# Optimization experiments

Measured on AMD Instinct MI355X. Metric: run time of the kernel, lower is better.

Reference implementation:

```python
import jax, jax.numpy as jnp
import numpy as np


def _to_complex(x):
    return x[..., 0] + 1j * x[..., 1]


def setup_inputs() -> dict:
    key = jax.random.key(0)
    ks = jax.random.split(key, 4)
    Bsz, L, D, N = 4, 16384, 512, 64
    u = jax.random.normal(ks[0], (Bsz, L, D), dtype=jnp.float32)
    # DPLR HiPPO-like init: real part -0.5, spread imaginary parts
    lam_re = -0.5 * jnp.ones((N,), jnp.float32)
    lam_im = jnp.pi * jnp.arange(N, dtype=jnp.float32)
    Lambda_ri = jnp.stack([lam_re, lam_im], axis=-1)              # (N, 2)
    P_ri = 0.5 * jax.random.normal(ks[1], (N, 2), jnp.float32)    # (N, 2)
    B_ri = 0.5 * jax.random.normal(ks[2], (N, D, 2), jnp.float32) # (N, D, 2)
    C_ri = (1.0 / np.float32(np.sqrt(N))) * jax.random.normal(ks[3], (1, N, 2), jnp.float32)
    D_param = jnp.ones((1,), jnp.float32)
    log_step = jnp.log(jnp.full((1,), 0.01, dtype=jnp.float32))
    return {"u": u, "Lambda_ri": Lambda_ri, "P_ri": P_ri, "B_ri": B_ri,
            "C_ri": C_ri, "D_param": D_param, "log_step": log_step}


def reference(u, Lambda_ri, P_ri, B_ri, C_ri, D_param, log_step):
    # Reassemble complex parameters (torch stores them via view_as_real)
    Lambda = _to_complex(Lambda_ri)   # (N,)
    P = _to_complex(P_ri)             # (N,)  (Q = P in S4Base)
    Bm = _to_complex(B_ri)            # (N, D)
    C = _to_complex(C_ri)             # (1, N)
    L = u.shape[-2]
    step = jnp.exp(log_step)[0]

    # --- conv_kernel_DPLR: Cauchy-kernel generating function at roots of unity ---
    Omega = jnp.exp((-2j * jnp.pi / L) * jnp.arange(L))          # (L,)
    g = (2.0 / step) * ((1.0 - Omega) / (1.0 + Omega))           # (L,)
    cauchy = 1.0 / (g[:, None] - Lambda[None, :])                # (L, N)
    aC = jnp.conj(C)[0]                                          # (N,)
    qc = jnp.conj(P)                                             # (N,)
    # k00[l,d] = sum_n C*[n] B[n,d] / (g[l]-Lambda[n]), etc.
    k00 = jnp.einsum('n,nd,ln->ld', aC, Bm, cauchy)              # (L, D)
    k01 = cauchy @ (aC * P)                                      # (L,)
    k10 = jnp.einsum('n,nd,ln->ld', qc, Bm, cauchy)              # (L, D)
    k11 = cauchy @ (qc * P)                                      # (L,)
    evaluated = (2.0 / (1.0 + Omega))[:, None] * (
        k00 - k01[:, None] * (1.0 / (1.0 + k11))[:, None] * k10)  # (L, D)
    K = jnp.fft.ifft(evaluated, n=L, axis=0).real                # (L, D) real kernel

    # --- convolve: FFT convolution over the sequence axis (zero-padded to 2L) ---
    n_fft = 2 * L
    ud = jnp.fft.rfft(u, n=n_fft, axis=-2)                       # (B, L+1..., D) complex
    Kd = jnp.fft.rfft(K, n=n_fft, axis=0)                        # (L+1..., D)
    y = jnp.fft.irfft(ud * Kd, n=n_fft, axis=-2)[..., :L, :]     # (B, L, D)
    return y + D_param * u
```

## Files before the change

kernel.cpp:

```cpp
#include <hip/hip_runtime.h>
#include <math.h>


#define D_DIM 512
#define NFFT 16384
#define TWO_PI_F 6.283185307179586f
#define PI_F 3.14159265358979323846f

struct C2 { float x, y; };

__device__ __forceinline__ C2 cmul(C2 a, C2 b){ return C2{a.x*b.x - a.y*b.y, a.x*b.y + a.y*b.x}; }
__device__ __forceinline__ C2 cadd(C2 a, C2 b){ return C2{a.x+b.x, a.y+b.y}; }
__device__ __forceinline__ C2 csub(C2 a, C2 b){ return C2{a.x-b.x, a.y-b.y}; }
__device__ __forceinline__ C2 cdiv(C2 a, C2 b){
  float inv = 1.f/(b.x*b.x + b.y*b.y);
  return C2{(a.x*b.x + a.y*b.y)*inv, (a.y*b.x - a.x*b.y)*inv};
}
__device__ __forceinline__ void cfma_(C2& acc, C2 a, C2 b){
  acc.x = fmaf(a.x, b.x, fmaf(-a.y, b.y, acc.x));
  acc.y = fmaf(a.x, b.y, fmaf( a.y, b.x, acc.y));
}

template<bool INV>
__device__ __forceinline__ void dft4(C2& a, C2& b, C2& c, C2& d){
  C2 t0 = cadd(a,c), t1 = csub(a,c), t2 = cadd(b,d), t3 = csub(b,d);
  C2 it3 = INV ? C2{-t3.y, t3.x} : C2{t3.y, -t3.x};
  a = cadd(t0,t2); c = csub(t0,t2); b = cadd(t1,it3); d = csub(t1,it3);
}

template<bool INV>
__device__ __forceinline__ void twd(C2& v, float c, float s){
  C2 w{c, INV ? s : -s};
  v = cmul(v, w);
}

template<bool INV>
__device__ __forceinline__ void dft16(C2 v[16]){
  dft4<INV>(v[0], v[4], v[8],  v[12]);
  dft4<INV>(v[1], v[5], v[9],  v[13]);
  dft4<INV>(v[2], v[6], v[10], v[14]);
  dft4<INV>(v[3], v[7], v[11], v[15]);
  const float C1 = 0.9238795325112867f, S1 = 0.3826834323650898f;
  const float CQ = 0.7071067811865476f;
  const float C3 = 0.3826834323650898f, S3 = 0.9238795325112867f;
  twd<INV>(v[5],  C1,  S1);
  twd<INV>(v[9],  CQ,  CQ);
  twd<INV>(v[13], C3,  S3);
  twd<INV>(v[6],  CQ,  CQ);
  twd<INV>(v[10], 0.f, 1.f);
  twd<INV>(v[14], -CQ, CQ);
  twd<INV>(v[7],  C3,  S3);
  twd<INV>(v[11], -CQ, CQ);
  twd<INV>(v[15], -C1, -S1);
  dft4<INV>(v[0],  v[1],  v[2],  v[3]);
  dft4<INV>(v[4],  v[5],  v[6],  v[7]);
  dft4<INV>(v[8],  v[9],  v[10], v[11]);
  dft4<INV>(v[12], v[13], v[14], v[15]);
}

template<bool INV>
__device__ __forceinline__ void dft8(C2 v[8]){
  C2 e0=v[0], e1=v[2], e2=v[4], e3=v[6];
  C2 o0=v[1], o1=v[3], o2=v[5], o3=v[7];
  dft4<INV>(e0,e1,e2,e3);
  dft4<INV>(o0,o1,o2,o3);
  const float r = 0.7071067811865476f;
  C2 w1 = INV ? C2{r, r}    : C2{r, -r};
  C2 w2 = INV ? C2{0.f,1.f} : C2{0.f,-1.f};
  C2 w3 = INV ? C2{-r, r}   : C2{-r, -r};
  C2 t0=o0, t1=cmul(o1,w1), t2=cmul(o2,w2), t3=cmul(o3,w3);
  v[0]=cadd(e0,t0); v[4]=csub(e0,t0);
  v[1]=cadd(e1,t1); v[5]=csub(e1,t1);
  v[2]=cadd(e2,t2); v[6]=csub(e2,t2);
  v[3]=cadd(e3,t3); v[7]=csub(e3,t3);
}

template<bool INV, bool PACK>
__global__ __launch_bounds__(256) void k_sweep1(const void* __restrict__ srcv, C2* __restrict__ out,
                                                long long src_bstride, long long out_bstride){
  __shared__ C2 V[128*32];
  int bx = blockIdx.x;
  int a  = bx & 127;
  int dt = bx >> 7;
  int tid = threadIdx.x;
  int dl = tid & 31;
  int g  = tid >> 5;
  int d0 = dt*32 + dl;
  const float sgn = INV ? 1.f : -1.f;
  C2* ob = out + (long long)blockIdx.y * out_bstride;

  #pragma unroll
  for (int h=0; h<2; ++h){
    int j1 = 2*g + h;
    C2 v[8];
    if constexpr (PACK){
      const float* sb = (const float*)srcv + (long long)blockIdx.y * src_bstride;
      #pragma unroll
      for (int j2=0;j2<4;j2++){
        int rr = a + 128*(j1 + 16*j2);
        v[j2].x = sb[(long long)(2*rr)  *D_DIM + d0];
        v[j2].y = sb[(long long)(2*rr+1)*D_DIM + d0];
      }
      #pragma unroll
      for (int j2=4;j2<8;j2++) v[j2] = C2{0.f,0.f};
    } else {
      const C2* sb = (const C2*)srcv + (long long)blockIdx.y * src_bstride;
      #pragma unroll
      for (int j2=0;j2<8;j2++){
        int rr = a + 128*(j1 + 16*j2);
        v[j2] = sb[(long long)rr*D_DIM + d0];
      }
    }
    dft8<INV>(v);
    float sn, cs; __sincosf(sgn * TWO_PI_F * (float)j1 * (1.f/128.f), &sn, &cs);
    C2 w1{cs, sn}; C2 w = w1;
    #pragma unroll
    for (int k2=1;k2<8;k2++){ v[k2] = cmul(v[k2], w); w = cmul(w, w1); }
    #pragma unroll
    for (int k2=0;k2<8;k2++) V[(k2*16 + j1)*32 + dl] = v[k2];
  }
  __syncthreads();
  C2 y[16];
  #pragma unroll
  for (int j1=0;j1<16;j1++) y[j1] = V[(g*16 + j1)*32 + dl];
  dft16<INV>(y);
  float sb_, cb_; __sincosf(sgn * TWO_PI_F * (float)(a*g) * (1.f/16384.f), &sb_, &cb_);
  float ss_, cs2; __sincosf(sgn * TWO_PI_F * (float)(8*a)  * (1.f/16384.f), &ss_, &cs2);
  C2 tw{cb_, sb_}; C2 stp{cs2, ss_};
  #pragma unroll
  for (int k1=0;k1<16;k1++){
    int pidx = ((k1&3)<<2) | (k1>>2);
    C2 val = cmul(y[pidx], tw);
    int k2p = g + 8*k1;
    ob[(long long)(k2p*128 + a)*D_DIM + d0] = val;
    tw = cmul(tw, stp);
  }
}

template<bool INV, int OMODE>
__global__ __launch_bounds__(256) void k_sweep2(const C2* __restrict__ in, void* __restrict__ outv,
                                                const float* __restrict__ u, const float* __restrict__ Dp,
                                                long long in_bstride, long long out_bstride){
  __shared__ C2 V[128*32];
  int bx = blockIdx.x;
  int a  = bx & 127;
  int dt = bx >> 7;
  int tid = threadIdx.x;
  int dl = tid & 31;
  int g  = tid >> 5;
  int d0 = dt*32 + dl;
  const float sgn = INV ? 1.f : -1.f;
  const C2* ib = in + (long long)blockIdx.y * in_bstride;

  #pragma unroll
  for (int h=0; h<2; ++h){
    int j1 = 2*g + h;
    C2 v[8];
    #pragma unroll
    for (int j2=0;j2<8;j2++){
      int rr = a*128 + (j1 + 16*j2);
      v[j2] = ib[(long long)rr*D_DIM + d0];
    }
    dft8<INV>(v);
    float sn, cs; __sincosf(sgn * TWO_PI_F * (float)j1 * (1.f/128.f), &sn, &cs);
    C2 w1{cs, sn}; C2 w = w1;
    #pragma unroll
    for (int k2=1;k2<8;k2++){ v[k2] = cmul(v[k2], w); w = cmul(w, w1); }
    #pragma unroll
    for (int k2=0;k2<8;k2++) V[(k2*16 + j1)*32 + dl] = v[k2];
  }
  __syncthreads();
  C2 y[16];
  #pragma unroll
  for (int j1=0;j1<16;j1++) y[j1] = V[(g*16 + j1)*32 + dl];
  dft16<INV>(y);
  #pragma unroll
  for (int k1=0;k1<16;k1++){
    int pidx = ((k1&3)<<2) | (k1>>2);
    C2 val = y[pidx];
    int row = a + 128*(g + 8*k1);
    if constexpr (OMODE == 0){
      C2* ob = (C2*)outv + (long long)blockIdx.y * out_bstride;
      ob[(long long)row*D_DIM + d0] = val;
    } else if constexpr (OMODE == 1){
      float* ob = (float*)outv;
      ob[(long long)row*D_DIM + d0] = val.x;
    } else {
      if (row < 8192){
        float* yb = (float*)outv + (long long)blockIdx.y * out_bstride;
        const float* ub = u + (long long)blockIdx.y * out_bstride;
        float dp = Dp[0];
        const float invN = 1.f/16384.f;
        yb[(long long)(2*row)  *D_DIM + d0] = fmaf(dp, ub[(long long)(2*row)  *D_DIM + d0], val.x*invN);
        yb[(long long)(2*row+1)*D_DIM + d0] = fmaf(dp, ub[(long long)(2*row+1)*D_DIM + d0], val.y*invN);
      }
    }
  }
}

__global__ __launch_bounds__(256) void k_mul(const C2* __restrict__ Zu, const C2* __restrict__ ZK,
                                             C2* __restrict__ Zp, long long bstride){
  int idx = blockIdx.x*256 + threadIdx.x;
  int d = idx & (D_DIM-1);
  int k = idx >> 9;
  int m = (NFFT - k) & (NFFT - 1);
  const C2* zub = Zu + (long long)blockIdx.y * bstride;
  C2*       zpb = Zp + (long long)blockIdx.y * bstride;
  C2 a  = zub[(long long)k*D_DIM + d];
  C2 bm = zub[(long long)m*D_DIM + d];
  C2 hk = ZK [(long long)k*D_DIM + d];
  C2 hm = ZK [(long long)m*D_DIM + d];
  float sw, cw; __sincosf(PI_F * (float)k / 16384.f, &sw, &cw);
  C2 w  { cw, -sw};
  C2 wm {-cw, -sw};
  C2 Ze  {0.5f*(a.x + bm.x), 0.5f*(a.y - bm.y)};
  C2 Zo  {0.5f*(a.y + bm.y), -0.5f*(a.x - bm.x)};
  C2 Xk = cadd(Ze, cmul(w, Zo));
  C2 Zem {0.5f*(bm.x + a.x), 0.5f*(bm.y - a.y)};
  C2 Zom {0.5f*(bm.y + a.y), -0.5f*(bm.x - a.x)};
  C2 Xm = cadd(Zem, cmul(wm, Zom));
  C2 KZe  {0.5f*(hk.x + hm.x), 0.5f*(hk.y - hm.y)};
  C2 KZo  {0.5f*(hk.y + hm.y), -0.5f*(hk.x - hm.x)};
  C2 Hk = cadd(KZe, cmul(w, KZo));
  C2 KZem {0.5f*(hm.x + hk.x), 0.5f*(hm.y - hk.y)};
  C2 KZom {0.5f*(hm.y + hk.y), -0.5f*(hm.x - hk.x)};
  C2 Hm = cadd(KZem, cmul(wm, KZom));
  C2 Yk = cmul(Xk, Hk);
  C2 Ym = cmul(Xm, Hm);
  C2 E  {0.5f*(Yk.x + Ym.x), 0.5f*(Yk.y - Ym.y)};
  C2 T  {0.5f*(Yk.x - Ym.x), 0.5f*(Yk.y + Ym.y)};
  C2 wp { cw, sw};
  C2 O = cmul(wp, T);
  zpb[(long long)k*D_DIM + d] = C2{E.x - O.y, E.y + O.x};
  if (k > 0 && k < 8192){
    C2 Em {0.5f*(Ym.x + Yk.x), 0.5f*(Ym.y - Yk.y)};
    C2 T2 {0.5f*(Ym.x - Yk.x), 0.5f*(Ym.y + Yk.y)};
    C2 wq {-cw, sw};
    C2 Om = cmul(wq, T2);
    zpb[(long long)m*D_DIM + d] = C2{Em.x - Om.y, Em.y + Om.x};
  }
}

__global__ __launch_bounds__(256) void k_prep(const float* __restrict__ B_ri, const float* __restrict__ C_ri,
                                              const float* __restrict__ P_ri,
                                              C2* __restrict__ U0, C2* __restrict__ U1, C2* __restrict__ vecs){
  int idx = blockIdx.x*256 + threadIdx.x;
  int n = idx >> 9;
  C2 Bnd { B_ri[2*idx], B_ri[2*idx+1] };
  C2 Cc  { C_ri[2*n], -C_ri[2*n+1] };
  C2 Pc  { P_ri[2*n], -P_ri[2*n+1] };
  U0[idx] = cmul(Cc, Bnd);
  U1[idx] = cmul(Pc, Bnd);
  if ((idx & (D_DIM-1)) == 0){
    C2 Pn { P_ri[2*n], P_ri[2*n+1] };
    vecs[n]       = cmul(Cc, Pn);
    vecs[64 + n]  = cmul(Pc, Pn);
  }
}

__global__ __launch_bounds__(256) void k_wprep(const float* __restrict__ Lambda_ri,
                                               const float* __restrict__ log_step,
                                               const C2* __restrict__ vecs,
                                               C2* __restrict__ Wbuf){
  __shared__ C2 p01[4][64];
  __shared__ C2 p11[4][64];
  __shared__ C2 sA1[64];
  int tid = threadIdx.x;
  int li = tid & 63, q = tid >> 6;
  int l = blockIdx.x*64 + li;
  float step = expf(log_step[0]);
  float ang = -TWO_PI_F * (float)l / 16384.f;
  float sn, cs; sincosf(ang, &sn, &cs);
  C2 den{1.f+cs, sn};
  C2 num{1.f-cs, -sn};
  C2 r = cdiv(num, den);
  float s2 = 2.f/step;
  C2 gl{r.x*s2, r.y*s2};
  C2 alpha = cdiv(C2{2.f/16384.f, 0.f}, den);
  C2 c[16]; C2 k01{0,0}, k11{0,0};
  #pragma unroll
  for (int i=0;i<16;i++){
    int n = q*16+i;
    C2 lam{Lambda_ri[2*n], Lambda_ri[2*n+1]};
    c[i] = cdiv(C2{1.f,0.f}, C2{gl.x-lam.x, gl.y-lam.y});
    cfma_(k01, c[i], vecs[n]);
    cfma_(k11, c[i], vecs[64+n]);
  }
  p01[q][li] = k01; p11[q][li] = k11;
  __syncthreads();
  if (q==0){
    C2 s01 = cadd(cadd(p01[0][li],p01[1][li]),cadd(p01[2][li],p01[3][li]));
    C2 s11 = cadd(cadd(p11[0][li],p11[1][li]),cadd(p11[2][li],p11[3][li]));
    C2 beta = cdiv(s01, C2{1.f+s11.x, s11.y});
    C2 ab = cmul(alpha, beta);
    sA1[li] = C2{-ab.x, -ab.y};
  }
  __syncthreads();
  C2 A1 = sA1[li];
  size_t base = (size_t)(l>>4)*(128*16) + (size_t)(l&15);
  #pragma unroll
  for (int i=0;i<16;i++){
    int n = q*16+i;
    Wbuf[base + (size_t)n*16]      = cmul(alpha, c[i]);
    Wbuf[base + (size_t)(64+n)*16] = cmul(A1, c[i]);
  }
}

__global__ __launch_bounds__(256) void k_ev2(const C2* __restrict__ U, const C2* __restrict__ Wbuf,
                                             C2* __restrict__ ev){
  int tid = threadIdx.x;
  int tile = blockIdx.x;
  int d0 = tid, d1 = tid + 256;
  const C2* __restrict__ Wt = Wbuf + (size_t)tile*(128*16);
  C2 acc0[16], acc1[16];
  #pragma unroll
  for (int li=0;li<16;li++){ acc0[li]=C2{0.f,0.f}; acc1[li]=C2{0.f,0.f}; }
  C2 u0 = U[d0], u1 = U[d1];
  for (int np=0; np<128; ++np){
    C2 nu0 = U[(size_t)(np+1)*D_DIM + d0];
    C2 nu1 = U[(size_t)(np+1)*D_DIM + d1];
    const C2* wr = Wt + (size_t)np*16;
    #pragma unroll
    for (int li=0;li<16;li++){
      C2 w = wr[li];
      cfma_(acc0[li], w, u0);
      cfma_(acc1[li], w, u1);
    }
    u0 = nu0; u1 = nu1;
  }
  long long l0 = (long long)tile*16;
  #pragma unroll
  for (int li=0;li<16;li++){
    ev[(l0+li)*D_DIM + d0] = acc0[li];
    ev[(l0+li)*D_DIM + d1] = acc1[li];
  }
}

extern "C" void kernel_launch(void* const* d_in, const int* in_sizes, int n_in,
                              void* d_out, int out_size, void* d_ws, size_t ws_size,
                              hipStream_t stream){
  const float* u         = (const float*)d_in[0];
  const float* Lambda_ri = (const float*)d_in[1];
  const float* P_ri      = (const float*)d_in[2];
  const float* B_ri      = (const float*)d_in[3];
  const float* C_ri      = (const float*)d_in[4];
  const float* Dp        = (const float*)d_in[5];
  const float* log_step  = (const float*)d_in[6];
  float* y = (float*)d_out;

  const long long ND = (long long)NFFT * D_DIM;
  const size_t SZ = (size_t)ND * sizeof(C2);

  int bc = 4;
  if (ws_size < (size_t)(2*4+1)*SZ) bc = 2;
  if (ws_size < (size_t)(2*2+1)*SZ) bc = 1;
  if (ws_size < (size_t)3*SZ) return;

  char* base = (char*)d_ws;
  C2* RA = (C2*)base;
  C2* RB = (C2*)(base + (size_t)bc*SZ);
  C2* RC = (C2*)(base + (size_t)2*bc*SZ);
  C2* Wbuf  = RC;
  float* Kreal = (float*)RC;
  C2* U0   = RB;
  C2* U1   = RB + 64*D_DIM;
  C2* vecs = RB + 2*64*D_DIM;
  C2* U    = RB;

  dim3 blk(256);

  k_prep <<<dim3(128),  blk, 0, stream>>>(B_ri, C_ri, P_ri, U0, U1, vecs);
  k_wprep<<<dim3(256),  blk, 0, stream>>>(Lambda_ri, log_step, vecs, Wbuf);
  k_ev2  <<<dim3(1024), blk, 0, stream>>>(U, Wbuf, RA);

  k_sweep1<true,false><<<dim3(2048,1), blk, 0, stream>>>(RA, RB, 0LL, 0LL);
  k_sweep2<true,1>    <<<dim3(2048,1), blk, 0, stream>>>(RB, Kreal, nullptr, nullptr, 0LL, 0LL);
  k_sweep1<false,true><<<dim3(2048,1), blk, 0, stream>>>(Kreal, RA, 0LL, 0LL);
  k_sweep2<false,0>   <<<dim3(2048,1), blk, 0, stream>>>(RA, RC, nullptr, nullptr, 0LL, 0LL);

  for (int b0 = 0; b0 < 4; b0 += bc){
    const float* ub = u + (long long)b0 * ND;
    float*       yb = y + (long long)b0 * ND;
    k_sweep1<false,true><<<dim3(2048,bc), blk, 0, stream>>>(ub, RA, ND, ND);
    k_sweep2<false,0>   <<<dim3(2048,bc), blk, 0, stream>>>(RA, RB, nullptr, nullptr, ND, ND);
    k_mul               <<<dim3(16386,bc), blk, 0, stream>>>(RB, RC, RA, ND);
    k_sweep1<true,false><<<dim3(2048,bc), blk, 0, stream>>>(RA, RB, ND, ND);
    k_sweep2<true,2>    <<<dim3(2048,bc), blk, 0, stream>>>(RB, yb, ub, Dp, ND, ND);
  }
}
```

Measured before the change: 845.8 us.

## Fuse spectral multiply into inverse FFT first pass; shrink ev2 L-tile

Removes the standalone k_mul kernel. Its real-FFT untangle and kernel multiply are now computed inside a new k_sweep1m kernel as it loads data for the inverse FFT's first pass, which saves a full round trip of the complex spectrum through global memory per batch. The cost is that each spectrum element's neighbour pair is read twice and the untangle arithmetic is done twice. Separately, the k_ev2 Cauchy evaluation tile shrinks from 16 to 8 sequence positions per block, with the grid doubled and the Wbuf layout in k_wprep changed to match, which halves accumulator registers for more occupancy at the cost of reading U twice as often.

```diff
diff --git a/kernel.cpp b/kernel.cpp
--- a/kernel.cpp
+++ b/kernel.cpp
@@ -137,6 +137,80 @@
   }
 }
 
+__global__ __launch_bounds__(256) void k_sweep1m(const C2* __restrict__ Zu, const C2* __restrict__ ZK,
+                                                 C2* __restrict__ out, long long bstride){
+  __shared__ C2 V[128*32];
+  int bx = blockIdx.x;
+  int a  = bx & 127;
+  int dt = bx >> 7;
+  int tid = threadIdx.x;
+  int dl = tid & 31;
+  int g  = tid >> 5;
+  int d0 = dt*32 + dl;
+  const C2* zub = Zu + (long long)blockIdx.y * bstride;
+  C2* ob = out + (long long)blockIdx.y * bstride;
+
+  #pragma unroll
+  for (int h=0; h<2; ++h){
+    int j1 = 2*g + h;
+    C2 v[8];
+    #pragma unroll
+    for (int j2=0;j2<8;j2++){
+      int rr = a + 128*(j1 + 16*j2);
+      int mr = (NFFT - rr) & (NFFT - 1);
+      C2 zk_ = zub[(long long)rr*D_DIM + d0];
+      C2 zm_ = zub[(long long)mr*D_DIM + d0];
+      C2 hk_ = ZK [(long long)rr*D_DIM + d0];
+      C2 hm_ = ZK [(long long)mr*D_DIM + d0];
+      float sw, cw; __sincosf(PI_F * (float)rr / 16384.f, &sw, &cw);
+      C2 w  { cw, -sw};
+      C2 wm {-cw, -sw};
+      C2 Ze  {0.5f*(zk_.x + zm_.x), 0.5f*(zk_.y - zm_.y)};
+      C2 Zo  {0.5f*(zk_.y + zm_.y), -0.5f*(zk_.x - zm_.x)};
+      C2 Xk = cadd(Ze, cmul(w, Zo));
+      C2 Zem {0.5f*(zm_.x + zk_.x), 0.5f*(zm_.y - zk_.y)};
+      C2 Zom {0.5f*(zm_.y + zk_.y), -0.5f*(zm_.x - zk_.x)};
+      C2 Xm = cadd(Zem, cmul(wm, Zom));
+      C2 KZe  {0.5f*(hk_.x + hm_.x), 0.5f*(hk_.y - hm_.y)};
+      C2 KZo  {0.5f*(hk_.y + hm_.y), -0.5f*(hk_.x - hm_.x)};
+      C2 Hk = cadd(KZe, cmul(w, KZo));
+      C2 KZem {0.5f*(hm_.x + hk_.x), 0.5f*(hm_.y - hk_.y)};
+      C2 KZom {0.5f*(hm_.y + hk_.y), -0.5f*(hm_.x - hk_.x)};
+      C2 Hm = cadd(KZem, cmul(wm, KZom));
+      C2 Yk = cmul(Xk, Hk);
+      C2 Ym = cmul(Xm, Hm);
+      C2 E  {0.5f*(Yk.x + Ym.x), 0.5f*(Yk.y - Ym.y)};
+      C2 T  {0.5f*(Yk.x - Ym.x), 0.5f*(Yk.y + Ym.y)};
+      C2 wp { cw, sw};
+      C2 O = cmul(wp, T);
+      v[j2] = C2{E.x - O.y, E.y + O.x};
+    }
+    dft8<true>(v);
+    float sn, cs; __sincosf(TWO_PI_F * (float)j1 * (1.f/128.f), &sn, &cs);
+    C2 w1{cs, sn}; C2 w = w1;
+    #pragma unroll
+    for (int k2=1;k2<8;k2++){ v[k2] = cmul(v[k2], w); w = cmul(w, w1); }
+    #pragma unroll
+    for (int k2=0;k2<8;k2++) V[(k2*16 + j1)*32 + dl] = v[k2];
+  }
+  __syncthreads();
+  C2 y[16];
+  #pragma unroll
+  for (int j1=0;j1<16;j1++) y[j1] = V[(g*16 + j1)*32 + dl];
+  dft16<true>(y);
+  float sb_, cb_; __sincosf(TWO_PI_F * (float)(a*g) * (1.f/16384.f), &sb_, &cb_);
+  float ss_, cs2; __sincosf(TWO_PI_F * (float)(8*a)  * (1.f/16384.f), &ss_, &cs2);
+  C2 tw{cb_, sb_}; C2 stp{cs2, ss_};
+  #pragma unroll
+  for (int k1=0;k1<16;k1++){
+    int pidx = ((k1&3)<<2) | (k1>>2);
+    C2 val = cmul(y[pidx], tw);
+    int k2p = g + 8*k1;
+    ob[(long long)(k2p*128 + a)*D_DIM + d0] = val;
+    tw = cmul(tw, stp);
+  }
+}
+
 template<bool INV, int OMODE>
 __global__ __launch_bounds__(256) void k_sweep2(const C2* __restrict__ in, void* __restrict__ outv,
                                                 const float* __restrict__ u, const float* __restrict__ Dp,
@@ -198,49 +272,6 @@
   }
 }
 
-__global__ __launch_bounds__(256) void k_mul(const C2* __restrict__ Zu, const C2* __restrict__ ZK,
-                                             C2* __restrict__ Zp, long long bstride){
-  int idx = blockIdx.x*256 + threadIdx.x;
-  int d = idx & (D_DIM-1);
-  int k = idx >> 9;
-  int m = (NFFT - k) & (NFFT - 1);
-  const C2* zub = Zu + (long long)blockIdx.y * bstride;
-  C2*       zpb = Zp + (long long)blockIdx.y * bstride;
-  C2 a  = zub[(long long)k*D_DIM + d];
-  C2 bm = zub[(long long)m*D_DIM + d];
-  C2 hk = ZK [(long long)k*D_DIM + d];
-  C2 hm = ZK [(long long)m*D_DIM + d];
-  float sw, cw; __sincosf(PI_F * (float)k / 16384.f, &sw, &cw);
-  C2 w  { cw, -sw};
-  C2 wm {-cw, -sw};
-  C2 Ze  {0.5f*(a.x + bm.x), 0.5f*(a.y - bm.y)};
-  C2 Zo  {0.5f*(a.y + bm.y), -0.5f*(a.x - bm.x)};
-  C2 Xk = cadd(Ze, cmul(w, Zo));
-  C2 Zem {0.5f*(bm.x + a.x), 0.5f*(bm.y - a.y)};
-  C2 Zom {0.5f*(bm.y + a.y), -0.5f*(bm.x - a.x)};
-  C2 Xm = cadd(Zem, cmul(wm, Zom));
-  C2 KZe  {0.5f*(hk.x + hm.x), 0.5f*(hk.y - hm.y)};
-  C2 KZo  {0.5f*(hk.y + hm.y), -0.5f*(hk.x - hm.x)};
-  C2 Hk = cadd(KZe, cmul(w, KZo));
-  C2 KZem {0.5f*(hm.x + hk.x), 0.5f*(hm.y - hk.y)};
-  C2 KZom {0.5f*(hm.y + hk.y), -0.5f*(hm.x - hk.x)};
-  C2 Hm = cadd(KZem, cmul(wm, KZom));
-  C2 Yk = cmul(Xk, Hk);
-  C2 Ym = cmul(Xm, Hm);
-  C2 E  {0.5f*(Yk.x + Ym.x), 0.5f*(Yk.y - Ym.y)};
-  C2 T  {0.5f*(Yk.x - Ym.x), 0.5f*(Yk.y + Ym.y)};
-  C2 wp { cw, sw};
-  C2 O = cmul(wp, T);
-  zpb[(long long)k*D_DIM + d] = C2{E.x - O.y, E.y + O.x};
-  if (k > 0 && k < 8192){
-    C2 Em {0.5f*(Ym.x + Yk.x), 0.5f*(Ym.y - Yk.y)};
-    C2 T2 {0.5f*(Ym.x - Yk.x), 0.5f*(Ym.y + Yk.y)};
-    C2 wq {-cw, sw};
-    C2 Om = cmul(wq, T2);
-    zpb[(long long)m*D_DIM + d] = C2{Em.x - Om.y, Em.y + Om.x};
-  }
-}
-
 __global__ __launch_bounds__(256) void k_prep(const float* __restrict__ B_ri, const float* __restrict__ C_ri,
                                               const float* __restrict__ P_ri,
                                               C2* __restrict__ U0, C2* __restrict__ U1, C2* __restrict__ vecs){
@@ -297,12 +328,12 @@
   }
   __syncthreads();
   C2 A1 = sA1[li];
-  size_t base = (size_t)(l>>4)*(128*16) + (size_t)(l&15);
+  size_t base = (size_t)(l>>3)*(128*8) + (size_t)(l&7);
   #pragma unroll
   for (int i=0;i<16;i++){
     int n = q*16+i;
-    Wbuf[base + (size_t)n*16]      = cmul(alpha, c[i]);
-    Wbuf[base + (size_t)(64+n)*16] = cmul(A1, c[i]);
+    Wbuf[base + (size_t)n*8]      = cmul(alpha, c[i]);
+    Wbuf[base + (size_t)(64+n)*8] = cmul(A1, c[i]);
   }
 }
 
@@ -311,26 +342,26 @@
   int tid = threadIdx.x;
   int tile = blockIdx.x;
   int d0 = tid, d1 = tid + 256;
-  const C2* __restrict__ Wt = Wbuf + (size_t)tile*(128*16);
-  C2 acc0[16], acc1[16];
-  #pragma unroll
-  for (int li=0;li<16;li++){ acc0[li]=C2{0.f,0.f}; acc1[li]=C2{0.f,0.f}; }
+  const C2* __restrict__ Wt = Wbuf + (size_t)tile*(128*8);
+  C2 acc0[8], acc1[8];
+  #pragma unroll
+  for (int li=0;li<8;li++){ acc0[li]=C2{0.f,0.f}; acc1[li]=C2{0.f,0.f}; }
   C2 u0 = U[d0], u1 = U[d1];
   for (int np=0; np<128; ++np){
     C2 nu0 = U[(size_t)(np+1)*D_DIM + d0];
     C2 nu1 = U[(size_t)(np+1)*D_DIM + d1];
-    const C2* wr = Wt + (size_t)np*16;
-    #pragma unroll
-    for (int li=0;li<16;li++){
+    const C2* wr = Wt + (size_t)np*8;
+    #pragma unroll
+    for (int li=0;li<8;li++){
       C2 w = wr[li];
       cfma_(acc0[li], w, u0);
       cfma_(acc1[li], w, u1);
     }
     u0 = nu0; u1 = nu1;
   }
-  long long l0 = (long long)tile*16;
-  #pragma unroll
-  for (int li=0;li<16;li++){
+  long long l0 = (long long)tile*8;
+  #pragma unroll
+  for (int li=0;li<8;li++){
     ev[(l0+li)*D_DIM + d0] = acc0[li];
     ev[(l0+li)*D_DIM + d1] = acc1[li];
   }
@@ -371,7 +402,7 @@
 
   k_prep <<<dim3(128),  blk, 0, stream>>>(B_ri, C_ri, P_ri, U0, U1, vecs);
   k_wprep<<<dim3(256),  blk, 0, stream>>>(Lambda_ri, log_step, vecs, Wbuf);
-  k_ev2  <<<dim3(1024), blk, 0, stream>>>(U, Wbuf, RA);
+  k_ev2  <<<dim3(2048), blk, 0, stream>>>(U, Wbuf, RA);
 
   k_sweep1<true,false><<<dim3(2048,1), blk, 0, stream>>>(RA, RB, 0LL, 0LL);
   k_sweep2<true,1>    <<<dim3(2048,1), blk, 0, stream>>>(RB, Kreal, nullptr, nullptr, 0LL, 0LL);
@@ -383,8 +414,7 @@
     float*       yb = y + (long long)b0 * ND;
     k_sweep1<false,true><<<dim3(2048,bc), blk, 0, stream>>>(ub, RA, ND, ND);
     k_sweep2<false,0>   <<<dim3(2048,bc), blk, 0, stream>>>(RA, RB, nullptr, nullptr, ND, ND);
-    k_mul               <<<dim3(16386,bc), blk, 0, stream>>>(RB, RC, RA, ND);
-    k_sweep1<true,false><<<dim3(2048,bc), blk, 0, stream>>>(RA, RB, ND, ND);
-    k_sweep2<true,2>    <<<dim3(2048,bc), blk, 0, stream>>>(RB, yb, ub, Dp, ND, ND);
-  }
-}
+    k_sweep1m           <<<dim3(2048,bc), blk, 0, stream>>>(RB, RC, RA, ND);
+    k_sweep2<true,2>    <<<dim3(2048,bc), blk, 0, stream>>>(RA, yb, ub, Dp, ND, ND);
+  }
+}
```

New measurement: 827.6 us. 2.2% less time.
